# Performance work log

Hardware: AMD Instinct MI355X
Metric: run time of the kernel (lower is better)

The kernel has to match this reference:

```python
import jax, jax.numpy as jnp
import numpy as np

NUM_CATEGORIES = 32
INPUT_DIM = 1536
HIDDEN_DIM = 1024
OUTPUT_DIM = 1024
B, T = 128, 32


def setup_inputs() -> dict:
    key = jax.random.key(0)
    k_x, k_cat, k_w1, k_w2 = jax.random.split(key, 4)
    x = jax.random.normal(k_x, (B, T, INPUT_DIM), dtype=jnp.float32)
    cat_ids = jax.random.randint(k_cat, (B,), 0, NUM_CATEGORIES)
    # CategorySpecificLinear params: W ~ 0.02*randn, b = zeros
    W1 = 0.02 * jax.random.normal(k_w1, (NUM_CATEGORIES, INPUT_DIM, HIDDEN_DIM), dtype=jnp.float32)
    b1 = jnp.zeros((NUM_CATEGORIES, HIDDEN_DIM), dtype=jnp.float32)
    W2 = 0.02 * jax.random.normal(k_w2, (NUM_CATEGORIES, HIDDEN_DIM, OUTPUT_DIM), dtype=jnp.float32)
    b2 = jnp.zeros((NUM_CATEGORIES, OUTPUT_DIM), dtype=jnp.float32)
    return {"x": x, "cat_ids": cat_ids, "W1": W1, "b1": b1, "W2": W2, "b2": b2}


def _cat_linear(x, W, b, cat_ids):
    # x: (B, T, D_in); W: (C, D_in, D_out); b: (C, D_out)
    # torch: bmm(x, W[cat_ids]) + b[cat_ids].unsqueeze(1)
    return jnp.einsum("btd,bdh->bth", x, W[cat_ids]) + b[cat_ids][:, None, :]


def reference(x, cat_ids, W1, b1, W2, b2):
    # CategorySpecificMLP.forward
    hidden = jax.nn.relu(_cat_linear(x, W1, b1, cat_ids))  # (B, T, H)
    return _cat_linear(hidden, W2, b2, cat_ids)            # (B, T, O)
```

## Files before the change

### kernel.cpp

```cpp
#include <hip/hip_runtime.h>
#include <hip/hip_bf16.h>
#include <stdint.h>

#define NCAT 32
#define DIN  1536
#define DMID 1024
#define NB   128
#define TT   32

#define BM 128
#define BN 64
#define BK 32
#define LDA 40
#define MAXG 56

typedef __attribute__((ext_vector_type(8))) short short8;
typedef __attribute__((ext_vector_type(4))) float f32x4;

static __device__ __forceinline__ unsigned int pk2bf(float lo, float hi) {
  unsigned short a = __builtin_bit_cast(unsigned short, __float2bfloat16(lo));
  unsigned short b = __builtin_bit_cast(unsigned short, __float2bfloat16(hi));
  return ((unsigned int)b << 16) | (unsigned int)a;
}

__global__ void build_groups(const int* __restrict__ cat_ids, int* __restrict__ wsi) {
  __shared__ int cats[NB];
  __shared__ int cnt[NCAT];
  __shared__ int off[NCAT];
  int t = threadIdx.x;
  cats[t] = cat_ids[t];
  __syncthreads();
  if (t < NCAT) {
    int n = 0;
    for (int b = 0; b < NB; b++) n += (cats[b] == t);
    cnt[t] = n;
  }
  __syncthreads();
  if (t == 0) {
    int acc = 0;
    for (int c = 0; c < NCAT; c++) { off[c] = acc; acc += cnt[c]; }
  }
  __syncthreads();
  if (t < NCAT) {
    int o = off[t];
    for (int b = 0; b < NB; b++)
      if (cats[b] == t) wsi[o++] = b;
  }
  if (t == 0) {
    for (int s = 0; s < MAXG; s++) {
      wsi[132 + s * 4 + 0] = 0;
      wsi[132 + s * 4 + 1] = 0;
      wsi[132 + s * 4 + 2] = 0;
    }
    int rload[8];
    for (int r = 0; r < 8; r++) rload[r] = 0;
    for (int c = 0; c < NCAT; c++) {
      int n = cnt[c];
      if (n == 0) continue;
      int o = off[c];
      int r = 0;
      for (int k = 1; k < 8; k++) if (rload[k] < rload[r]) r = k;
      for (int j = 0; j < n; j += 4) {
        if (rload[r] >= 7) {
          r = 0;
          for (int k = 1; k < 8; k++) if (rload[k] < rload[r]) r = k;
        }
        int s = r + 8 * rload[r];
        rload[r]++;
        wsi[132 + s * 4 + 0] = c;
        wsi[132 + s * 4 + 1] = o + j;
        wsi[132 + s * 4 + 2] = (n - j) < 4 ? (n - j) : 4;
      }
    }
    wsi[128] = MAXG;
  }
}

template <int LAYER>
__global__ __launch_bounds__(256)
void mlp_gemm(const void* __restrict__ Ain, const float* __restrict__ W,
              const float* __restrict__ bias, const int* __restrict__ wsi,
              void* __restrict__ Out, int K) {
  const int l    = blockIdx.y * 16 + blockIdx.x;
  const int xcd  = l & 7;
  const int m    = l >> 3;
  const int slot = xcd + 8 * (m >> 4);
  const int cat   = wsi[132 + slot * 4 + 0];
  const int start = wsi[132 + slot * 4 + 1];
  const int cnt   = wsi[132 + slot * 4 + 2];
  if (cnt == 0) return;
  const int n0 = (m & 15) * BN;

  __shared__ unsigned short As[BM * LDA];
  __shared__ unsigned short Bs[4 * BN * 8];

  const int tid  = threadIdx.x;
  const int lane = tid & 63;
  const int w    = tid >> 6;

  const int arow  = tid >> 1;
  const int khalf = (tid & 1) * 16;
  const int lb    = arow >> 5;
  const int tok   = arow & 31;
  const int lbc   = lb < (cnt - 1) ? lb : (cnt - 1);
  const int batch = wsi[start + lbc];
  const long grow = (long)(batch * TT + tok);

  const float* Wcol = W + (size_t)cat * (size_t)K * 1024 + n0 + lane;

  f32x4 acc[4][2];
#pragma unroll
  for (int i = 0; i < 4; i++)
#pragma unroll
    for (int j = 0; j < 2; j++) acc[i][j] = (f32x4){0.f, 0.f, 0.f, 0.f};

  const int wm  = (w >> 1) * 64;
  const int wn  = (w & 1) * 32;
  const int kg  = lane >> 4;
  const int c16 = lane & 15;

  auto load_tile = [&](int k0, float4 ar[4], uint4& ah0, uint4& ah1, float br[8]) {
    if constexpr (LAYER == 1) {
      const float* ap = (const float*)Ain + grow * (long)K + k0 + khalf;
      ar[0] = *(const float4*)(ap + 0);
      ar[1] = *(const float4*)(ap + 4);
      ar[2] = *(const float4*)(ap + 8);
      ar[3] = *(const float4*)(ap + 12);
    } else {
      const uint4* ap = (const uint4*)((const unsigned short*)Ain + grow * (long)K + k0 + khalf);
      ah0 = ap[0];
      ah1 = ap[1];
    }
    const float* bp = Wcol + (size_t)(k0 + w * 8) * 1024;
#pragma unroll
    for (int r = 0; r < 8; r++) br[r] = bp[(size_t)r * 1024];
  };

  auto store_tile = [&](const float4 ar[4], const uint4& ah0, const uint4& ah1,
                        const float br[8]) {
    if constexpr (LAYER == 1) {
      uint4 aw0 = make_uint4(pk2bf(ar[0].x, ar[0].y), pk2bf(ar[0].z, ar[0].w),
                             pk2bf(ar[1].x, ar[1].y), pk2bf(ar[1].z, ar[1].w));
      uint4 aw1 = make_uint4(pk2bf(ar[2].x, ar[2].y), pk2bf(ar[2].z, ar[2].w),
                             pk2bf(ar[3].x, ar[3].y), pk2bf(ar[3].z, ar[3].w));
      *(uint4*)&As[arow * LDA + khalf]     = aw0;
      *(uint4*)&As[arow * LDA + khalf + 8] = aw1;
    } else {
      *(uint4*)&As[arow * LDA + khalf]     = ah0;
      *(uint4*)&As[arow * LDA + khalf + 8] = ah1;
    }
    uint4 bw = make_uint4(pk2bf(br[0], br[1]), pk2bf(br[2], br[3]),
                          pk2bf(br[4], br[5]), pk2bf(br[6], br[7]));
    *(uint4*)&Bs[(w * BN + lane) * 8] = bw;
  };

  float4 arC[4]; uint4 ah0C, ah1C; float brC[8];
  load_tile(0, arC, ah0C, ah1C, brC);

  for (int k0 = 0; k0 < K; k0 += BK) {
    float4 arN[4]; uint4 ah0N, ah1N; float brN[8];
    const bool more = (k0 + BK < K);
    if (more) load_tile(k0 + BK, arN, ah0N, ah1N, brN);

    __syncthreads();
    store_tile(arC, ah0C, ah1C, brC);
    __syncthreads();

    short8 afrag[4], bfrag[2];
#pragma unroll
    for (int i = 0; i < 4; i++)
      afrag[i] = *(const short8*)&As[(wm + i * 16 + c16) * LDA + kg * 8];
#pragma unroll
    for (int j = 0; j < 2; j++)
      bfrag[j] = *(const short8*)&Bs[(kg * BN + wn + j * 16 + c16) * 8];
#pragma unroll
    for (int i = 0; i < 4; i++)
#pragma unroll
      for (int j = 0; j < 2; j++)
        acc[i][j] = __builtin_amdgcn_mfma_f32_16x16x32_bf16(afrag[i], bfrag[j], acc[i][j], 0, 0, 0);

    if (more) {
#pragma unroll
      for (int i = 0; i < 4; i++) arC[i] = arN[i];
      ah0C = ah0N; ah1C = ah1N;
#pragma unroll
      for (int r = 0; r < 8; r++) brC[r] = brN[r];
    }
  }

  const int rquad = (lane >> 4) * 4;
#pragma unroll
  for (int i = 0; i < 4; i++) {
#pragma unroll
    for (int j = 0; j < 2; j++) {
      int gcol = n0 + wn + j * 16 + c16;
      float bb = bias[cat * 1024 + gcol];
#pragma unroll
      for (int r = 0; r < 4; r++) {
        int lrow = wm + i * 16 + rquad + r;
        int lb2 = lrow >> 5;
        if (lb2 < cnt) {
          int b2 = wsi[start + lb2];
          long orow = (long)(b2 * TT + (lrow & 31));
          float v = acc[i][j][r] + bb;
          if constexpr (LAYER == 1) {
            v = fmaxf(v, 0.f);
            ((unsigned short*)Out)[orow * DMID + gcol] =
                __builtin_bit_cast(unsigned short, __float2bfloat16(v));
          } else {
            ((float*)Out)[orow * 1024 + gcol] = v;
          }
        }
      }
    }
  }
}

extern "C" void kernel_launch(void* const* d_in, const int* in_sizes, int n_in,
                              void* d_out, int out_size, void* d_ws, size_t ws_size,
                              hipStream_t stream) {
  const float* x       = (const float*)d_in[0];
  const int*   cat_ids = (const int*)d_in[1];
  const float* W1      = (const float*)d_in[2];
  const float* b1      = (const float*)d_in[3];
  const float* W2      = (const float*)d_in[4];
  const float* b2      = (const float*)d_in[5];
  float* out = (float*)d_out;

  int* wsi = (int*)d_ws;
  unsigned short* hidden = (unsigned short*)((char*)d_ws + 8192);

  build_groups<<<dim3(1), dim3(128), 0, stream>>>(cat_ids, wsi);
  mlp_gemm<1><<<dim3(1024 / BN, MAXG), dim3(256), 0, stream>>>(
      (const void*)x, W1, b1, wsi, (void*)hidden, DIN);
  mlp_gemm<2><<<dim3(1024 / BN, MAXG), dim3(256), 0, stream>>>(
      (const void*)hidden, W2, b2, wsi, (void*)out, DMID);
}
```

Before: 449.3 us.

## Double-buffer LDS tiles with two-deep register prefetch and single barrier

Splits the A and B shared-memory tiles into two buffers and unrolls the K loop by two, so each iteration stores the next tile into the other buffer while computing on the current one. This needs only one barrier per tile instead of two. It also keeps two register tiles in flight to prefetch further ahead, and uses a custom barrier that waits only on LDS counters, so pending global loads are not drained at each barrier. The cost is more LDS and registers, which may reduce occupancy, and the loop assumes the tile count is even.

Measured after the change: 486.3 us. 8.2% more time.

```diff
diff --git a/kernel.cpp b/kernel.cpp
--- a/kernel.cpp
+++ b/kernel.cpp
@@ -21,6 +21,12 @@
   unsigned short a = __builtin_bit_cast(unsigned short, __float2bfloat16(lo));
   unsigned short b = __builtin_bit_cast(unsigned short, __float2bfloat16(hi));
   return ((unsigned int)b << 16) | (unsigned int)a;
+}
+
+static __device__ __forceinline__ void bar_noflush() {
+  asm volatile("s_waitcnt lgkmcnt(0)" ::: "memory");
+  __builtin_amdgcn_s_barrier();
+  asm volatile("" ::: "memory");
 }
 
 __global__ void build_groups(const int* __restrict__ cat_ids, int* __restrict__ wsi) {
@@ -91,8 +97,8 @@
   if (cnt == 0) return;
   const int n0 = (m & 15) * BN;
 
-  __shared__ unsigned short As[BM * LDA];
-  __shared__ unsigned short Bs[4 * BN * 8];
+  __shared__ unsigned short As[2][BM * LDA];
+  __shared__ unsigned short Bs[2][4 * BN * 8];
 
   const int tid  = threadIdx.x;
   const int lane = tid & 63;
@@ -119,7 +125,7 @@
   const int kg  = lane >> 4;
   const int c16 = lane & 15;
 
-  auto load_tile = [&](int k0, float4 ar[4], uint4& ah0, uint4& ah1, float br[8]) {
+  auto load_tile = [&](int k0, float4 ar[4], uint4 ah[2], float br[8]) {
     if constexpr (LAYER == 1) {
       const float* ap = (const float*)Ain + grow * (long)K + k0 + khalf;
       ar[0] = *(const float4*)(ap + 0);
@@ -128,64 +134,66 @@
       ar[3] = *(const float4*)(ap + 12);
     } else {
       const uint4* ap = (const uint4*)((const unsigned short*)Ain + grow * (long)K + k0 + khalf);
-      ah0 = ap[0];
-      ah1 = ap[1];
+      ah[0] = ap[0];
+      ah[1] = ap[1];
     }
     const float* bp = Wcol + (size_t)(k0 + w * 8) * 1024;
 #pragma unroll
     for (int r = 0; r < 8; r++) br[r] = bp[(size_t)r * 1024];
   };
 
-  auto store_tile = [&](const float4 ar[4], const uint4& ah0, const uint4& ah1,
-                        const float br[8]) {
+  auto store_tile = [&](int buf, const float4 ar[4], const uint4 ah[2], const float br[8]) {
     if constexpr (LAYER == 1) {
       uint4 aw0 = make_uint4(pk2bf(ar[0].x, ar[0].y), pk2bf(ar[0].z, ar[0].w),
                              pk2bf(ar[1].x, ar[1].y), pk2bf(ar[1].z, ar[1].w));
       uint4 aw1 = make_uint4(pk2bf(ar[2].x, ar[2].y), pk2bf(ar[2].z, ar[2].w),
                              pk2bf(ar[3].x, ar[3].y), pk2bf(ar[3].z, ar[3].w));
-      *(uint4*)&As[arow * LDA + khalf]     = aw0;
-      *(uint4*)&As[arow * LDA + khalf + 8] = aw1;
+      *(uint4*)&As[buf][arow * LDA + khalf]     = aw0;
+      *(uint4*)&As[buf][arow * LDA + khalf + 8] = aw1;
     } else {
-      *(uint4*)&As[arow * LDA + khalf]     = ah0;
-      *(uint4*)&As[arow * LDA + khalf + 8] = ah1;
+      *(uint4*)&As[buf][arow * LDA + khalf]     = ah[0];
+      *(uint4*)&As[buf][arow * LDA + khalf + 8] = ah[1];
     }
     uint4 bw = make_uint4(pk2bf(br[0], br[1]), pk2bf(br[2], br[3]),
                           pk2bf(br[4], br[5]), pk2bf(br[6], br[7]));
-    *(uint4*)&Bs[(w * BN + lane) * 8] = bw;
+    *(uint4*)&Bs[buf][(w * BN + lane) * 8] = bw;
   };
 
-  float4 arC[4]; uint4 ah0C, ah1C; float brC[8];
-  load_tile(0, arC, ah0C, ah1C, brC);
-
-  for (int k0 = 0; k0 < K; k0 += BK) {
-    float4 arN[4]; uint4 ah0N, ah1N; float brN[8];
-    const bool more = (k0 + BK < K);
-    if (more) load_tile(k0 + BK, arN, ah0N, ah1N, brN);
-
-    __syncthreads();
-    store_tile(arC, ah0C, ah1C, brC);
-    __syncthreads();
-
+  auto compute = [&](int buf) {
     short8 afrag[4], bfrag[2];
 #pragma unroll
     for (int i = 0; i < 4; i++)
-      afrag[i] = *(const short8*)&As[(wm + i * 16 + c16) * LDA + kg * 8];
+      afrag[i] = *(const short8*)&As[buf][(wm + i * 16 + c16) * LDA + kg * 8];
 #pragma unroll
     for (int j = 0; j < 2; j++)
-      bfrag[j] = *(const short8*)&Bs[(kg * BN + wn + j * 16 + c16) * 8];
+      bfrag[j] = *(const short8*)&Bs[buf][(kg * BN + wn + j * 16 + c16) * 8];
 #pragma unroll
     for (int i = 0; i < 4; i++)
 #pragma unroll
       for (int j = 0; j < 2; j++)
         acc[i][j] = __builtin_amdgcn_mfma_f32_16x16x32_bf16(afrag[i], bfrag[j], acc[i][j], 0, 0, 0);
-
-    if (more) {
-#pragma unroll
-      for (int i = 0; i < 4; i++) arC[i] = arN[i];
-      ah0C = ah0N; ah1C = ah1N;
-#pragma unroll
-      for (int r = 0; r < 8; r++) brC[r] = brN[r];
-    }
+  };
+
+  float4 arA[4]; uint4 ahA[2]; float brA[8];
+  float4 arB[4]; uint4 ahB[2]; float brB[8];
+
+  const int nt = K / BK;
+
+  load_tile(0, arA, ahA, brA);
+  load_tile(BK, arB, ahB, brB);
+  store_tile(0, arA, ahA, brA);
+  bar_noflush();
+
+  for (int t = 0; t + 2 <= nt; t += 2) {
+    if (t + 2 < nt) load_tile((t + 2) * BK, arA, ahA, brA);
+    store_tile(1, arB, ahB, brB);
+    compute(0);
+    bar_noflush();
+
+    if (t + 3 < nt) load_tile((t + 3) * BK, arB, ahB, brB);
+    if (t + 2 < nt) store_tile(0, arA, ahA, brA);
+    compute(1);
+    bar_noflush();
   }
 
   const int rquad = (lane >> 4) * 4;
```
